# Kernel tuning notes

Hardware: AMD Instinct MI355X
Metric: run time of the kernel (lower is better)

The kernel has to match this reference:

```python
import jax, jax.numpy as jnp
import numpy as np

B, H, W = 1, 32, 32
C, G, K = 128, 4, 15
GC = C // G          # group channels = 32
K2 = K * K           # 225
RED = 4              # SE reduction
KHID = 32            # kernel_net hidden


def setup_inputs() -> dict:
    key = jax.random.key(0)
    ks = jax.random.split(key, 24)
    def n(k, shape, s=0.02):
        return jax.random.normal(k, shape, jnp.float32) * s
    inp = {
        'x': jax.random.normal(ks[0], (B, H, W, C), jnp.float32),
        # scalars (torch: raw_sigma init = softplus^{-1}(0.3), base_offset_scale = 0.1)
        'raw_sigma': jnp.asarray(float(np.log(np.expm1(0.3))), jnp.float32),
        'base_offset_scale': jnp.asarray(0.1, jnp.float32),
        # input/output projections
        'w_in': n(ks[1], (C, C)), 'b_in': jnp.zeros((C,), jnp.float32),
        'w_out': n(ks[2], (C, C)), 'b_out': jnp.zeros((C,), jnp.float32),
        # dw_conv: depthwise 3x3 (HWIO, I=1 per group) + pointwise 1x1
        'dw_k': n(ks[3], (3, 3, 1, C), 0.1), 'dw_b': jnp.zeros((C,), jnp.float32),
        'pw_w': n(ks[4], (C, C)), 'pw_b': jnp.zeros((C,), jnp.float32),
        # offset / mask nets (zero-init in torch; small random here to exercise gather)
        'off_w': n(ks[5], (C, G * K2 * 2), 0.01), 'off_b': n(ks[6], (G * K2 * 2,), 0.01),
        'msk_w': n(ks[7], (C, G * K2), 0.01), 'msk_b': n(ks[8], (G * K2,), 0.01),
        # kernel_net: 2 -> 32 -> 32 -> G*GC
        'k1_w': n(ks[9], (2, KHID), 0.3), 'k1_b': jnp.zeros((KHID,), jnp.float32),
        'k2_w': n(ks[10], (KHID, KHID), 0.2), 'k2_b': jnp.zeros((KHID,), jnp.float32),
        'k3_w': n(ks[11], (KHID, G * GC), 0.2), 'k3_b': jnp.zeros((G * GC,), jnp.float32),
        # SE block
        'se1_w': n(ks[12], (C, C // RED), 0.1), 'se1_b': jnp.zeros((C // RED,), jnp.float32),
        'se2_w': n(ks[13], (C // RED, C), 0.1), 'se2_b': jnp.zeros((C,), jnp.float32),
    }
    return inp


def reference(x, raw_sigma, base_offset_scale, w_in, b_in, w_out, b_out,
              dw_k, dw_b, pw_w, pw_b, off_w, off_b, msk_w, msk_b,
              k1_w, k1_b, k2_w, k2_b, k3_w, k3_b, se1_w, se1_b, se2_w, se2_b):
    # sigma (scalar path, biases=None)
    sigma = jnp.clip(jax.nn.softplus(raw_sigma), 0.001, 0.5)
    grid = jnp.linspace(-0.5, 0.5, K)

    x_proj = x @ w_in + b_in                                   # [B,H,W,C]

    # dw_conv: depthwise 3x3 -> SiLU -> 1x1
    y = jax.lax.conv_general_dilated(
        x, dw_k, (1, 1), 'SAME',
        dimension_numbers=('NHWC', 'HWIO', 'NHWC'),
        feature_group_count=C) + dw_b
    x_dw = jax.nn.silu(y) @ pw_w + pw_b                        # [B,H,W,C]

    # Gaussian envelope over kernel grid, normalized (scalar sigma -> shape [K,K])
    gh = grid[:, None]; gw = grid[None, :]
    env = jnp.exp(-(gh ** 2 + gw ** 2) / (2.0 * sigma ** 2))
    env = env / jnp.clip(env.sum(), 1e-8)                      # [K,K]

    # dynamic kernel weights from grid positions (*2); replicate torch's
    # contiguous view (K,K,G,gc) -> (G,K2,gc)
    pos = jnp.stack(jnp.meshgrid(grid, grid, indexing='ij'), -1).reshape(K2, 2) * 2.0
    h1 = jax.nn.silu(pos @ k1_w + k1_b)
    h2 = jax.nn.silu(h1 @ k2_w + k2_b)
    kw = (h2 @ k3_w + k3_b).reshape(K, K, G, GC).reshape(G, K2, GC)  # [G,K2,gc]

    offsets = (x_dw @ off_w + off_b).reshape(B, H, W, G, K2, 2) * base_offset_scale
    raw_mask = (x_dw @ msk_w + msk_b).reshape(B, H, W, G, K2) * env.reshape(1, 1, 1, 1, K2)
    attn = jnp.nan_to_num(jax.nn.softmax(raw_mask, axis=-1))   # [B,H,W,G,K2]

    # reference sampling grid (integer offsets -K//2..K//2)
    ref = jnp.linspace(-(K // 2), K // 2, K)
    ref_grid = jnp.stack(jnp.meshgrid(ref, ref, indexing='ij'), -1).reshape(K2, 2)
    pos_h = jnp.arange(H, dtype=jnp.float32).reshape(1, H, 1, 1, 1)
    pos_w = jnp.arange(W, dtype=jnp.float32).reshape(1, 1, W, 1, 1)

    abs_h = pos_h + ref_grid[:, 0].reshape(1, 1, 1, 1, K2) + offsets[..., 0]
    abs_w = pos_w + ref_grid[:, 1].reshape(1, 1, 1, 1, K2) + offsets[..., 1]
    ah = jnp.clip(abs_h, 0.0, H - 1); aw = jnp.clip(abs_w, 0.0, W - 1)
    hf = jnp.clip(ah.astype(jnp.int32), 0, H - 1)
    wf = jnp.clip(aw.astype(jnp.int32), 0, W - 1)
    hc = jnp.clip(hf + 1, 0, H - 1)
    wc = jnp.clip(wf + 1, 0, W - 1)
    hw = ah - hf.astype(jnp.float32)
    ww = aw - wf.astype(jnp.float32)
    valid = (~((abs_h < 0) | (abs_h > H - 1) | (abs_w < 0) | (abs_w > W - 1))).astype(jnp.float32)

    x_g = x_proj.reshape(B, H, W, G, GC)
    b_idx = jnp.arange(B).reshape(B, 1, 1, 1, 1)
    g_idx = jnp.arange(G).reshape(1, 1, 1, G, 1)
    def gather(hi, wi):
        return x_g[b_idx, hi, wi, g_idx]                       # [B,H,W,G,K2,gc]

    sampled = (gather(hf, wf) * ((1 - hw) * (1 - ww) * valid)[..., None]
             + gather(hf, wc) * ((1 - hw) * ww * valid)[..., None]
             + gather(hc, wf) * (hw * (1 - ww) * valid)[..., None]
             + gather(hc, wc) * (hw * ww * valid)[..., None])

    sampled = sampled * kw.reshape(1, 1, 1, G, K2, GC)
    out = jnp.einsum('bhwgkc,bhwgk->bhwgc', sampled, attn).reshape(B, H, W, C)

    # SE block (mask=None, bias=None)
    pooled = out.mean(axis=(1, 2), keepdims=True)
    scale = jax.nn.sigmoid(jax.nn.silu(pooled @ se1_w + se1_b) @ se2_w + se2_b)
    out = out * scale

    return out @ w_out + b_out
```

## Files before the change

### kernel.cpp

```cpp
#include <hip/hip_runtime.h>
#include <math.h>

constexpr int H = 32, W = 32, C = 128, G = 4, K = 15, K2 = 225, GC = 32;
constexpr int NPIX = H * W;
constexpr int NOFF = G * K2 * 2;
constexpr int NMSK = G * K2;
constexpr int NTOT = NOFF + NMSK;
constexpr int KHID = 32;

constexpr size_t WS_ENV    = 128;
constexpr size_t WS_KW     = 384;
constexpr size_t WS_PART   = 29184;
constexpr size_t WS_XPROJ  = 94720;
constexpr size_t WS_XDW    = 225792;
constexpr size_t WS_OFFS   = 356864;
constexpr size_t WS_MASK   = 2200064;
constexpr size_t WS_OUTPRE = 3121664;

__device__ __forceinline__ float sigmoidf_(float v) { return 1.f / (1.f + expf(-v)); }
__device__ __forceinline__ float siluf_(float v)    { return v / (1.f + expf(-v)); }

__device__ __forceinline__ unsigned short f2bf(float f) {
    unsigned u = __float_as_uint(f);
    unsigned r = u + 0x7FFFu + ((u >> 16) & 1u);
    return (unsigned short)(r >> 16);
}
__device__ __forceinline__ float bf2f(unsigned short u) {
    return __uint_as_float((unsigned)u << 16);
}

__device__ __forceinline__ void mlp_point(int k2i, int lane,
        const float* __restrict__ k1_w, const float* __restrict__ k1_b,
        const float* __restrict__ k2_w, const float* __restrict__ k2_b,
        const float* __restrict__ k3_w, const float* __restrict__ k3_b,
        float* __restrict__ ws) {
    int i = k2i / 15, j = k2i % 15;
    float ph = (-0.5f + (float)i * (1.f / 14.f)) * 2.f;
    float pw = (-0.5f + (float)j * (1.f / 14.f)) * 2.f;
    float h1[KHID], h2[KHID];
#pragma unroll
    for (int m = 0; m < KHID; m++)
        h1[m] = siluf_(fmaf(ph, k1_w[m], fmaf(pw, k1_w[KHID + m], k1_b[m])));
#pragma unroll
    for (int m = 0; m < KHID; m++) {
        float a = k2_b[m];
#pragma unroll
        for (int q = 0; q < KHID; q++) a = fmaf(h1[q], k2_w[q * KHID + m], a);
        h2[m] = siluf_(a);
    }
#pragma unroll
    for (int t = 0; t < 2; t++) {
        int col = lane + t * 64;
        float a = k3_b[col];
#pragma unroll
        for (int q = 0; q < KHID; q++) a = fmaf(h2[q], k3_w[q * C + col], a);
        ws[WS_KW + (size_t)k2i * C + col] = a;
    }
}

__global__ __launch_bounds__(256) void prep_front_kernel(const float* __restrict__ x,
        const float* __restrict__ raw_sigma,
        const float* __restrict__ w_in, const float* __restrict__ b_in,
        const float* __restrict__ dw_k, const float* __restrict__ dw_b,
        const float* __restrict__ pw_w, const float* __restrict__ pw_b,
        const float* __restrict__ k1_w, const float* __restrict__ k1_b,
        const float* __restrict__ k2_w, const float* __restrict__ k2_b,
        const float* __restrict__ k3_w, const float* __restrict__ k3_b,
        float* __restrict__ ws) {
    int tid = threadIdx.x;
    int b = blockIdx.x;
    if (b < 256) {
        __shared__ float xs[4][C], ts[4][C];
        unsigned short* xph = (unsigned short*)(ws + WS_XPROJ);
        int p0 = b * 4;
        int c = tid & 127, pp = tid >> 7;
#pragma unroll
        for (int q = 0; q < 2; q++) {
            int px = pp * 2 + q;
            int p = p0 + px;
            int h = p >> 5, w = p & 31;
            xs[px][c] = x[(size_t)p * C + c];
            float y = dw_b[c];
#pragma unroll
            for (int dy = 0; dy < 3; dy++) {
                int hh = h + dy - 1;
                if (hh < 0 || hh >= H) continue;
#pragma unroll
                for (int dx = 0; dx < 3; dx++) {
                    int wq = w + dx - 1;
                    if (wq < 0 || wq >= W) continue;
                    y = fmaf(x[((size_t)hh * W + wq) * C + c], dw_k[(dy * 3 + dx) * C + c], y);
                }
            }
            ts[px][c] = siluf_(y);
        }
        __syncthreads();
        float ap0 = b_in[c], ap1 = ap0, ad0 = pw_b[c], ad1 = ad0;
        int b0 = pp * 2, b1 = pp * 2 + 1;
        for (int i = 0; i < C; i += 4) {
#pragma unroll
            for (int u = 0; u < 4; u++) {
                float wi = w_in[(size_t)(i + u) * C + c];
                float pi = pw_w[(size_t)(i + u) * C + c];
                ap0 = fmaf(xs[b0][i + u], wi, ap0);
                ap1 = fmaf(xs[b1][i + u], wi, ap1);
                ad0 = fmaf(ts[b0][i + u], pi, ad0);
                ad1 = fmaf(ts[b1][i + u], pi, ad1);
            }
        }
        xph[(size_t)(p0 + b0) * C + c] = f2bf(ap0);
        xph[(size_t)(p0 + b1) * C + c] = f2bf(ap1);
        ws[WS_XDW  + (size_t)(p0 + b0) * C + c] = ad0;
        ws[WS_XDW  + (size_t)(p0 + b1) * C + c] = ad1;
    } else {
        int mb = b - 256;
        if (mb == 0) {
            __shared__ float red[256];
            float xsg = raw_sigma[0];
            float sp = fmaxf(xsg, 0.f) + log1pf(expf(-fabsf(xsg)));
            float sigma = fminf(fmaxf(sp, 0.001f), 0.5f);
            float inv2s2 = 1.f / (2.f * sigma * sigma);
            int i = tid / 15, j = tid % 15;
            float e = 0.f;
            if (tid < K2) {
                float gi = -0.5f + (float)i * (1.f / 14.f);
                float gj = -0.5f + (float)j * (1.f / 14.f);
                e = expf(-(gi * gi + gj * gj) * inv2s2);
            }
            red[tid] = e;
            __syncthreads();
            for (int s = 128; s > 0; s >>= 1) {
                if (tid < s) red[tid] += red[tid + s];
                __syncthreads();
            }
            float esum = fmaxf(red[0], 1e-8f);
            if (tid < K2) ws[WS_ENV + tid] = e / esum;
            if (tid < 64) mlp_point(224, tid, k1_w, k1_b, k2_w, k2_b, k3_w, k3_b, ws);
        } else {
            int k2i = (mb - 1) * 4 + (tid >> 6);
            mlp_point(k2i, tid & 63, k1_w, k1_b, k2_w, k2_b, k3_w, k3_b, ws);
        }
    }
}

__global__ __launch_bounds__(256) void offmsk_gemm(const float* __restrict__ A,
        const float* __restrict__ off_w, const float* __restrict__ off_b,
        const float* __restrict__ msk_w, const float* __restrict__ msk_b,
        const float* __restrict__ bos, const float* __restrict__ env,
        float* __restrict__ offs_out, float* __restrict__ mask_out) {
    __shared__ float At[32][72];
    __shared__ float Bs[32][64];
    int tid = threadIdx.x;
    int c0 = blockIdx.x * 64;
    int p0 = blockIdx.y * 64;
    int tx = tid & 15, ty = tid >> 4;
    float acc[4][4];
#pragma unroll
    for (int i = 0; i < 4; i++)
#pragma unroll
        for (int j = 0; j < 4; j++) acc[i][j] = 0.f;
    int cL = (tid * 4) & 63;
    int kL = (tid * 4) >> 6;
    int cB = c0 + cL;
    const float* bptr = nullptr; int bstride = 0;
    if (cB < NOFF)       { bptr = off_w + cB;          bstride = NOFF; }
    else if (cB < NTOT)  { bptr = msk_w + (cB - NOFF); bstride = NMSK; }
    int rA = tid >> 3, k4A = (tid & 7) * 4;
    for (int kt = 0; kt < C; kt += 32) {
        if (kt) __syncthreads();
#pragma unroll
        for (int pass = 0; pass < 2; pass++) {
            int r = rA + pass * 32;
            float4 v = *(const float4*)&A[(size_t)(p0 + r) * C + kt + k4A];
            At[k4A + 0][r] = v.x; At[k4A + 1][r] = v.y;
            At[k4A + 2][r] = v.z; At[k4A + 3][r] = v.w;
            int k = kL + pass * 16;
            float4 bv = make_float4(0.f, 0.f, 0.f, 0.f);
            if (bptr) bv = *(const float4*)&bptr[(size_t)(kt + k) * bstride];
            *(float4*)&Bs[k][cL] = bv;
        }
        __syncthreads();
#pragma unroll
        for (int k = 0; k < 32; k++) {
            float4 a4 = *(const float4*)&At[k][ty * 4];
            float4 b4 = *(const float4*)&Bs[k][tx * 4];
            const float av[4] = {a4.x, a4.y, a4.z, a4.w};
            const float bv[4] = {b4.x, b4.y, b4.z, b4.w};
#pragma unroll
            for (int i = 0; i < 4; i++)
#pragma unroll
                for (int j = 0; j < 4; j++)
                    acc[i][j] = fmaf(av[i], bv[j], acc[i][j]);
        }
    }
    int colbase = c0 + tx * 4;
    if (colbase >= NTOT) return;
    float bias[4], sc[4];
    float* obase; int ostride;
    if (colbase < NOFF) {
        float s = bos[0];
#pragma unroll
        for (int j = 0; j < 4; j++) { bias[j] = off_b[colbase + j]; sc[j] = s; }
        obase = offs_out + colbase; ostride = NOFF;
    } else {
        int m0 = colbase - NOFF;
#pragma unroll
        for (int j = 0; j < 4; j++) { bias[j] = msk_b[m0 + j]; sc[j] = env[(m0 + j) % K2]; }
        obase = mask_out + m0; ostride = NMSK;
    }
#pragma unroll
    for (int i = 0; i < 4; i++) {
        size_t row = (size_t)(p0 + ty * 4 + i);
        float4 r0 = make_float4((acc[i][0] + bias[0]) * sc[0], (acc[i][1] + bias[1]) * sc[1],
                                (acc[i][2] + bias[2]) * sc[2], (acc[i][3] + bias[3]) * sc[3]);
        *(float4*)&obase[row * ostride] = r0;
    }
}

__global__ __launch_bounds__(256, 8) void sampler_kernel(const float* __restrict__ ws_offs,
        const float* __restrict__ ws_mask, const unsigned short* __restrict__ xprojh,
        const float* __restrict__ kwf, float* __restrict__ outpre,
        float* __restrict__ partial) {
    int blk = blockIdx.x;
    int pp = blk >> 2;
    int g  = blk & 3;
    int p0 = pp * 2;
    int h = p0 >> 5;
    int tid = threadIdx.x;

    __shared__ float   attn_s[2][K2];
    __shared__ float4  wgt_s[2][K2];
    __shared__ ushort4 loc_s[2][K2];
    __shared__ float4  rbuf[16][16];

    if (tid < 128) {
        int px = tid >> 6, lane = tid & 63;
        const float* mrow = ws_mask + (size_t)(p0 + px) * NMSK + g * K2;
        float v[4];
        float mx = -1e30f;
#pragma unroll
        for (int q = 0; q < 4; q++) {
            int k = lane + q * 64;
            v[q] = (k < K2) ? mrow[k] : -1e30f;
            mx = fmaxf(mx, v[q]);
        }
#pragma unroll
        for (int s = 32; s > 0; s >>= 1) mx = fmaxf(mx, __shfl_xor(mx, s));
        float sum = 0.f;
#pragma unroll
        for (int q = 0; q < 4; q++) {
            int k = lane + q * 64;
            v[q] = (k < K2) ? expf(v[q] - mx) : 0.f;
            sum += v[q];
        }
#pragma unroll
        for (int s = 32; s > 0; s >>= 1) sum += __shfl_xor(sum, s);
        float inv = 1.f / sum;
#pragma unroll
        for (int q = 0; q < 4; q++) {
            int k = lane + q * 64;
            if (k < K2) attn_s[px][k] = v[q] * inv;
        }
    }
    __syncthreads();

    for (int e = tid; e < 2 * K2; e += 256) {
        int px = (e >= K2) ? 1 : 0;
        int k = e - px * K2;
        int p = p0 + px;
        int w = p & 31;
        float2 o = *(const float2*)&ws_offs[(size_t)p * NOFF + (g * K2 + k) * 2];
        float abs_h = (float)(h + k / 15 - 7) + o.x;
        float abs_w = (float)(w + k % 15 - 7) + o.y;
        float validf = (abs_h < 0.f || abs_h > 31.f || abs_w < 0.f || abs_w > 31.f) ? 0.f : 1.f;
        float ah = fminf(fmaxf(abs_h, 0.f), 31.f);
        float aw = fminf(fmaxf(abs_w, 0.f), 31.f);
        int hf = (int)ah, wf = (int)aw;
        int hc = min(hf + 1, 31), wc = min(wf + 1, 31);
        float hwt = ah - (float)hf, wwt = aw - (float)wf;
        float a = attn_s[px][k] * validf;
        float u0 = 1.f - hwt, u1 = 1.f - wwt;
        wgt_s[px][k] = make_float4(a * u0 * u1, a * u0 * wwt, a * hwt * u1, a * hwt * wwt);
        loc_s[px][k] = make_ushort4((unsigned short)(hf * W + wf), (unsigned short)(hf * W + wc),
                                    (unsigned short)(hc * W + wf), (unsigned short)(hc * W + wc));
    }
    __syncthreads();

    {
        int cq = tid & 7;
        int px = (tid >> 3) & 1;
        int s  = tid >> 4;
        int k0 = s * 15;
        int k1 = min(k0 + 15, K2);
        const unsigned short* xpg = xprojh + g * GC + cq * 4;
        const float* kwg = kwf + (size_t)g * (K2 * GC) + cq * 4;
        float4 acc = make_float4(0.f, 0.f, 0.f, 0.f);
        for (int k = k0; k < k1; k++) {
            float4 Wv = wgt_s[px][k];
            if (Wv.x + Wv.y + Wv.z + Wv.w == 0.f) continue;
            ushort4 L = loc_s[px][k];
            ushort4 u00 = *(const ushort4*)(xpg + (size_t)L.x * C);
            ushort4 u01 = *(const ushort4*)(xpg + (size_t)L.y * C);
            ushort4 u10 = *(const ushort4*)(xpg + (size_t)L.z * C);
            ushort4 u11 = *(const ushort4*)(xpg + (size_t)L.w * C);
            float4 kw4 = *(const float4*)(kwg + k * GC);
            float sx = fmaf(Wv.w, bf2f(u11.x), fmaf(Wv.z, bf2f(u10.x),
                       fmaf(Wv.y, bf2f(u01.x), Wv.x * bf2f(u00.x))));
            float sy = fmaf(Wv.w, bf2f(u11.y), fmaf(Wv.z, bf2f(u10.y),
                       fmaf(Wv.y, bf2f(u01.y), Wv.x * bf2f(u00.y))));
            float sz = fmaf(Wv.w, bf2f(u11.z), fmaf(Wv.z, bf2f(u10.z),
                       fmaf(Wv.y, bf2f(u01.z), Wv.x * bf2f(u00.z))));
            float sw = fmaf(Wv.w, bf2f(u11.w), fmaf(Wv.z, bf2f(u10.w),
                       fmaf(Wv.y, bf2f(u01.w), Wv.x * bf2f(u00.w))));
            acc.x = fmaf(kw4.x, sx, acc.x);
            acc.y = fmaf(kw4.y, sy, acc.y);
            acc.z = fmaf(kw4.z, sz, acc.z);
            acc.w = fmaf(kw4.w, sw, acc.w);
        }
        rbuf[s][px * 8 + cq] = acc;
    }
    __syncthreads();

    if (tid < 64) {
        int px = tid >> 5, cc = tid & 31;
        int cq = cc >> 2, j = cc & 3;
        float v = 0.f;
#pragma unroll
        for (int s = 0; s < 16; s++)
            v += ((const float*)&rbuf[s][px * 8 + cq])[j];
        outpre[(size_t)(p0 + px) * C + g * GC + cc] = v;
        float pv = v + __shfl_xor(v, 32);
        if (px == 0)
            partial[(size_t)pp * C + g * GC + cc] = pv;
    }
}

__global__ __launch_bounds__(256) void finale_kernel(const float* __restrict__ outpre,
        const float* __restrict__ partial,
        const float* __restrict__ se1_w, const float* __restrict__ se1_b,
        const float* __restrict__ se2_w, const float* __restrict__ se2_b,
        const float* __restrict__ w_out, const float* __restrict__ b_out,
        float* __restrict__ out) {
    int tid = threadIdx.x;
    __shared__ float tmp[8][132];
    __shared__ float pooled[C];
    __shared__ float hid[KHID];
    __shared__ float scl[C];
    __shared__ float v[4][C];

    {
        int bg = tid >> 5, c4 = (tid & 31) * 4;
        float4 s4 = make_float4(0.f, 0.f, 0.f, 0.f);
        for (int i = 0; i < 64; i++) {
            float4 pv = *(const float4*)&partial[(size_t)(bg * 64 + i) * C + c4];
            s4.x += pv.x; s4.y += pv.y; s4.z += pv.z; s4.w += pv.w;
        }
        *(float4*)&tmp[bg][c4] = s4;
    }
    __syncthreads();
    if (tid < C) {
        float s = 0.f;
#pragma unroll
        for (int g = 0; g < 8; g++) s += tmp[g][tid];
        pooled[tid] = s * (1.f / 1024.f);
    }
    __syncthreads();
    if (tid < KHID) {
        float a = se1_b[tid];
        for (int cc = 0; cc < C; cc++) a = fmaf(pooled[cc], se1_w[cc * KHID + tid], a);
        hid[tid] = siluf_(a);
    }
    __syncthreads();
    if (tid < C) {
        float a = se2_b[tid];
#pragma unroll
        for (int q = 0; q < KHID; q++) a = fmaf(hid[q], se2_w[q * C + tid], a);
        scl[tid] = sigmoidf_(a);
    }
    __syncthreads();

    int p0 = blockIdx.x * 4;
    int c = tid & 127, pp = tid >> 7;
#pragma unroll
    for (int q = 0; q < 2; q++) {
        int px = pp * 2 + q;
        v[px][c] = outpre[(size_t)(p0 + px) * C + c] * scl[c];
    }
    __syncthreads();
    float a0 = b_out[c], a1 = b_out[c];
    int b0 = pp * 2, b1 = pp * 2 + 1;
    for (int i = 0; i < C; i += 4) {
#pragma unroll
        for (int u = 0; u < 4; u++) {
            float wv = w_out[(size_t)(i + u) * C + c];
            a0 = fmaf(v[b0][i + u], wv, a0);
            a1 = fmaf(v[b1][i + u], wv, a1);
        }
    }
    out[(size_t)(p0 + b0) * C + c] = a0;
    out[(size_t)(p0 + b1) * C + c] = a1;
}

extern "C" void kernel_launch(void* const* d_in, const int* in_sizes, int n_in,
                              void* d_out, int out_size, void* d_ws, size_t ws_size,
                              hipStream_t stream) {
    const float* x         = (const float*)d_in[0];
    const float* raw_sigma = (const float*)d_in[1];
    const float* bos       = (const float*)d_in[2];
    const float* w_in      = (const float*)d_in[3];
    const float* b_in      = (const float*)d_in[4];
    const float* w_out     = (const float*)d_in[5];
    const float* b_out     = (const float*)d_in[6];
    const float* dw_k      = (const float*)d_in[7];
    const float* dw_b      = (const float*)d_in[8];
    const float* pw_w      = (const float*)d_in[9];
    const float* pw_b      = (const float*)d_in[10];
    const float* off_w     = (const float*)d_in[11];
    const float* off_b     = (const float*)d_in[12];
    const float* msk_w     = (const float*)d_in[13];
    const float* msk_b     = (const float*)d_in[14];
    const float* k1_w      = (const float*)d_in[15];
    const float* k1_b      = (const float*)d_in[16];
    const float* k2_w      = (const float*)d_in[17];
    const float* k2_b      = (const float*)d_in[18];
    const float* k3_w      = (const float*)d_in[19];
    const float* k3_b      = (const float*)d_in[20];
    const float* se1_w     = (const float*)d_in[21];
    const float* se1_b     = (const float*)d_in[22];
    const float* se2_w     = (const float*)d_in[23];
    const float* se2_b     = (const float*)d_in[24];

    float* ws  = (float*)d_ws;
    float* out = (float*)d_out;

    prep_front_kernel<<<313, 256, 0, stream>>>(x, raw_sigma, w_in, b_in, dw_k, dw_b,
                                               pw_w, pw_b, k1_w, k1_b, k2_w, k2_b,
                                               k3_w, k3_b, ws);

    dim3 gg((NTOT + 63) / 64, NPIX / 64);
    offmsk_gemm<<<gg, 256, 0, stream>>>(ws + WS_XDW, off_w, off_b, msk_w, msk_b, bos,
                                        ws + WS_ENV, ws + WS_OFFS, ws + WS_MASK);

    sampler_kernel<<<NPIX * 2, 256, 0, stream>>>(ws + WS_OFFS, ws + WS_MASK,
                                                 (const unsigned short*)(ws + WS_XPROJ),
                                                 ws + WS_KW, ws + WS_OUTPRE, ws + WS_PART);

    finale_kernel<<<NPIX / 4, 256, 0, stream>>>(ws + WS_OUTPRE, ws + WS_PART,
                                                se1_w, se1_b, se2_w, se2_b,
                                                w_out, b_out, out);
}
```

Measured before the change: 67.06 us.

## Use split-bf16 MFMA for offset/mask projection GEMM

Replaces the scalar FP32 register-tiled GEMM that computes offsets and masks with a matrix-core version. Each FP32 operand is split into a high and a low bf16 part, and three bf16 MFMA products (hi*hi, lo*hi, hi*lo) approximate FP32 accuracy. The goal is to cut FMA throughput cost on the largest GEMM (1024x2700x128). In exchange it adds conversion work and transposed, strided single-float B loads into shared memory, and the output stores become scalar strided writes instead of float4.

```diff
diff --git a/kernel.cpp b/kernel.cpp
--- a/kernel.cpp
+++ b/kernel.cpp
@@ -16,6 +16,9 @@
 constexpr size_t WS_OFFS   = 356864;
 constexpr size_t WS_MASK   = 2200064;
 constexpr size_t WS_OUTPRE = 3121664;
+
+typedef short bf16x8 __attribute__((ext_vector_type(8)));
+typedef float f32x4  __attribute__((ext_vector_type(4)));
 
 __device__ __forceinline__ float sigmoidf_(float v) { return 1.f / (1.f + expf(-v)); }
 __device__ __forceinline__ float siluf_(float v)    { return v / (1.f + expf(-v)); }
@@ -110,8 +113,8 @@
         }
         xph[(size_t)(p0 + b0) * C + c] = f2bf(ap0);
         xph[(size_t)(p0 + b1) * C + c] = f2bf(ap1);
-        ws[WS_XDW  + (size_t)(p0 + b0) * C + c] = ad0;
-        ws[WS_XDW  + (size_t)(p0 + b1) * C + c] = ad1;
+        ws[WS_XDW + (size_t)(p0 + b0) * C + c] = ad0;
+        ws[WS_XDW + (size_t)(p0 + b1) * C + c] = ad1;
     } else {
         int mb = b - 256;
         if (mb == 0) {
@@ -143,77 +146,101 @@
     }
 }
 
-__global__ __launch_bounds__(256) void offmsk_gemm(const float* __restrict__ A,
+__global__ __launch_bounds__(256) void offmsk_gemm_mfma(const float* __restrict__ xdw,
         const float* __restrict__ off_w, const float* __restrict__ off_b,
         const float* __restrict__ msk_w, const float* __restrict__ msk_b,
         const float* __restrict__ bos, const float* __restrict__ env,
         float* __restrict__ offs_out, float* __restrict__ mask_out) {
-    __shared__ float At[32][72];
-    __shared__ float Bs[32][64];
+    __shared__ __align__(16) unsigned short As_hi[64][72];
+    __shared__ __align__(16) unsigned short As_lo[64][72];
+    __shared__ __align__(16) unsigned short Bs_hi[64][72];
+    __shared__ __align__(16) unsigned short Bs_lo[64][72];
     int tid = threadIdx.x;
     int c0 = blockIdx.x * 64;
     int p0 = blockIdx.y * 64;
-    int tx = tid & 15, ty = tid >> 4;
-    float acc[4][4];
-#pragma unroll
-    for (int i = 0; i < 4; i++)
-#pragma unroll
-        for (int j = 0; j < 4; j++) acc[i][j] = 0.f;
-    int cL = (tid * 4) & 63;
-    int kL = (tid * 4) >> 6;
-    int cB = c0 + cL;
-    const float* bptr = nullptr; int bstride = 0;
-    if (cB < NOFF)       { bptr = off_w + cB;          bstride = NOFF; }
-    else if (cB < NTOT)  { bptr = msk_w + (cB - NOFF); bstride = NMSK; }
-    int rA = tid >> 3, k4A = (tid & 7) * 4;
-    for (int kt = 0; kt < C; kt += 32) {
-        if (kt) __syncthreads();
-#pragma unroll
-        for (int pass = 0; pass < 2; pass++) {
-            int r = rA + pass * 32;
-            float4 v = *(const float4*)&A[(size_t)(p0 + r) * C + kt + k4A];
-            At[k4A + 0][r] = v.x; At[k4A + 1][r] = v.y;
-            At[k4A + 2][r] = v.z; At[k4A + 3][r] = v.w;
-            int k = kL + pass * 16;
-            float4 bv = make_float4(0.f, 0.f, 0.f, 0.f);
-            if (bptr) bv = *(const float4*)&bptr[(size_t)(kt + k) * bstride];
-            *(float4*)&Bs[k][cL] = bv;
+
+    int w = tid >> 6, l = tid & 63;
+    int lr = l & 15, lk8 = (l >> 4) * 8;
+
+    int n = tid & 63;
+    int col = c0 + n;
+    bool bvalid = col < NTOT;
+    const float* wsrc = off_w + (bvalid && col < NOFF ? col : 0);
+    int wstr = NOFF;
+    if (bvalid && col >= NOFF) { wsrc = msk_w + (col - NOFF); wstr = NMSK; }
+
+    f32x4 acc[4];
+#pragma unroll
+    for (int j = 0; j < 4; j++) acc[j] = (f32x4){0.f, 0.f, 0.f, 0.f};
+
+    for (int kc = 0; kc < C; kc += 64) {
+        if (kc) __syncthreads();
+        {
+            int r = tid >> 2, kq = (tid & 3) * 16;
+#pragma unroll
+            for (int i = 0; i < 4; i++) {
+                float4 v = *(const float4*)&xdw[(size_t)(p0 + r) * C + kc + kq + i * 4];
+                const float* vf = (const float*)&v;
+#pragma unroll
+                for (int u = 0; u < 4; u++) {
+                    unsigned short hh = f2bf(vf[u]);
+                    As_hi[r][kq + i * 4 + u] = hh;
+                    As_lo[r][kq + i * 4 + u] = f2bf(vf[u] - bf2f(hh));
+                }
+            }
+        }
+        {
+            int kg = tid >> 6;
+#pragma unroll
+            for (int i = 0; i < 16; i++) {
+                int k = kg * 16 + i;
+                float f = bvalid ? wsrc[(size_t)(kc + k) * wstr] : 0.f;
+                unsigned short hh = f2bf(f);
+                Bs_hi[n][k] = hh;
+                Bs_lo[n][k] = f2bf(f - bf2f(hh));
+            }
         }
         __syncthreads();
-#pragma unroll
-        for (int k = 0; k < 32; k++) {
-            float4 a4 = *(const float4*)&At[k][ty * 4];
-            float4 b4 = *(const float4*)&Bs[k][tx * 4];
-            const float av[4] = {a4.x, a4.y, a4.z, a4.w};
-            const float bv[4] = {b4.x, b4.y, b4.z, b4.w};
-#pragma unroll
-            for (int i = 0; i < 4; i++)
-#pragma unroll
-                for (int j = 0; j < 4; j++)
-                    acc[i][j] = fmaf(av[i], bv[j], acc[i][j]);
-        }
-    }
-    int colbase = c0 + tx * 4;
-    if (colbase >= NTOT) return;
-    float bias[4], sc[4];
-    float* obase; int ostride;
-    if (colbase < NOFF) {
-        float s = bos[0];
-#pragma unroll
-        for (int j = 0; j < 4; j++) { bias[j] = off_b[colbase + j]; sc[j] = s; }
-        obase = offs_out + colbase; ostride = NOFF;
-    } else {
-        int m0 = colbase - NOFF;
-#pragma unroll
-        for (int j = 0; j < 4; j++) { bias[j] = msk_b[m0 + j]; sc[j] = env[(m0 + j) % K2]; }
-        obase = mask_out + m0; ostride = NMSK;
-    }
-#pragma unroll
-    for (int i = 0; i < 4; i++) {
-        size_t row = (size_t)(p0 + ty * 4 + i);
-        float4 r0 = make_float4((acc[i][0] + bias[0]) * sc[0], (acc[i][1] + bias[1]) * sc[1],
-                                (acc[i][2] + bias[2]) * sc[2], (acc[i][3] + bias[3]) * sc[3]);
-        *(float4*)&obase[row * ostride] = r0;
+
+        bf16x8 a_hi[2], a_lo[2];
+#pragma unroll
+        for (int ks = 0; ks < 2; ks++) {
+            a_hi[ks] = *(const bf16x8*)&As_hi[w * 16 + lr][ks * 32 + lk8];
+            a_lo[ks] = *(const bf16x8*)&As_lo[w * 16 + lr][ks * 32 + lk8];
+        }
+#pragma unroll
+        for (int j = 0; j < 4; j++) {
+#pragma unroll
+            for (int ks = 0; ks < 2; ks++) {
+                bf16x8 b_hi = *(const bf16x8*)&Bs_hi[j * 16 + lr][ks * 32 + lk8];
+                bf16x8 b_lo = *(const bf16x8*)&Bs_lo[j * 16 + lr][ks * 32 + lk8];
+                acc[j] = __builtin_amdgcn_mfma_f32_16x16x32_bf16(a_hi[ks], b_hi, acc[j], 0, 0, 0);
+                acc[j] = __builtin_amdgcn_mfma_f32_16x16x32_bf16(a_lo[ks], b_hi, acc[j], 0, 0, 0);
+                acc[j] = __builtin_amdgcn_mfma_f32_16x16x32_bf16(a_hi[ks], b_lo, acc[j], 0, 0, 0);
+            }
+        }
+    }
+
+#pragma unroll
+    for (int j = 0; j < 4; j++) {
+        int ocol = c0 + j * 16 + lr;
+        if (ocol < NTOT) {
+            float bias, sc;
+            float* obase;
+            int ostr;
+            if (ocol < NOFF) {
+                bias = off_b[ocol]; sc = bos[0];
+                obase = offs_out + ocol; ostr = NOFF;
+            } else {
+                int m0 = ocol - NOFF;
+                bias = msk_b[m0]; sc = env[m0 % K2];
+                obase = mask_out + m0; ostr = NMSK;
+            }
+            int row0 = p0 + w * 16 + (l >> 4) * 4;
+#pragma unroll
+            for (int r = 0; r < 4; r++)
+                obase[(size_t)(row0 + r) * ostr] = (acc[j][r] + bias) * sc;
+        }
     }
 }
 
@@ -438,8 +465,8 @@
                                                k3_w, k3_b, ws);
 
     dim3 gg((NTOT + 63) / 64, NPIX / 64);
-    offmsk_gemm<<<gg, 256, 0, stream>>>(ws + WS_XDW, off_w, off_b, msk_w, msk_b, bos,
-                                        ws + WS_ENV, ws + WS_OFFS, ws + WS_MASK);
+    offmsk_gemm_mfma<<<gg, 256, 0, stream>>>(ws + WS_XDW, off_w, off_b, msk_w, msk_b,
+                                             bos, ws + WS_ENV, ws + WS_OFFS, ws + WS_MASK);
 
     sampler_kernel<<<NPIX * 2, 256, 0, stream>>>(ws + WS_OFFS, ws + WS_MASK,
                                                  (const unsigned short*)(ws + WS_XPROJ),
```

Result: no change. 67.94 us (+1.3%).
